# Performance work log

Hardware: AMD Instinct MI355X
Metric: run time of the kernel (lower is better)

Reference implementation:

```python
import jax, jax.numpy as jnp
import numpy as np

ENC_H = 512
DEC_H = 512
FIELD = 128

def setup_inputs() -> dict:
    key = jax.random.key(0)
    ks = jax.random.split(key, 12)
    B, S, T = 8, 256, 32
    def lin(k, fan_in, fan_out):
        k1, k2 = jax.random.split(k)
        bound = 1.0 / np.sqrt(fan_in)
        W = jax.random.uniform(k1, (fan_in, fan_out), minval=-bound, maxval=bound, dtype=jnp.float32)
        b = jax.random.uniform(k2, (fan_out,), minval=-bound, maxval=bound, dtype=jnp.float32)
        return W, b
    W1, b1 = lin(ks[0], ENC_H, DEC_H)
    W2, b2 = lin(ks[1], DEC_H, DEC_H)
    W3, b3 = lin(ks[2], FIELD, DEC_H)
    W4, b4 = lin(ks[3], DEC_H, DEC_H)
    return {
        "output": jax.random.normal(ks[4], (B, T, DEC_H), dtype=jnp.float32),
        "encoder_hidden": jax.random.normal(ks[5], (S, B, ENC_H), dtype=jnp.float32),
        "input_z": jax.random.normal(ks[6], (B, S, FIELD), dtype=jnp.float32),
        "W1": W1, "b1": b1, "W2": W2, "b2": b2,
        "W3": W3, "b3": b3, "W4": W4, "b4": b4,
    }

def reference(output, encoder_hidden, input_z, W1, b1, W2, b2, W3, b3, W4, b4):
    S, B, He = encoder_hidden.shape
    # tanh(lin1(encoder_hidden)) then .view(B, S, D)  (reshape, NOT transpose -- faithful to torch .view)
    out_hs = jnp.tanh(encoder_hidden @ W1 + b1).reshape(B, S, -1)      # [B,S,D]
    enc_h = encoder_hidden.reshape(B, S, He)                            # [B,S,He]
    out_fds = jnp.tanh(input_z @ W3 + b3)                               # [B,S,D]
    out2 = jnp.tanh(output @ W2 + b2)                                   # [B,T,D]
    out3 = jnp.tanh(output @ W4 + b4)                                   # [B,T,D]
    # vectorized over timesteps: g1[b,s,t,d] = out_hs[b,s,d]*out2[b,t,d]
    g1 = out_hs[:, :, None, :] * out2[:, None, :, :]                    # [B,S,T,D]
    alpha = jax.nn.softmax(g1, axis=1)                                  # softmax over S, per feature d
    g2 = out_fds[:, :, None, :] * out3[:, None, :, :]                   # [B,S,T,D]
    beta = jax.nn.softmax(g2, axis=1)
    q = alpha * beta                                                    # [B,S,T,D]
    qn = jax.lax.stop_gradient(jnp.sum(q, axis=1, keepdims=True))       # detached normalizer
    gamma = q / qn                                                      # [B,S,T,D]
    contex = jnp.sum(gamma * enc_h[:, :, None, :], axis=1)              # [B,T,D]
    concat_vectors = jnp.concatenate([output, contex], axis=-1)         # [B,T,2D]
    # attn: list over t of gamma[:, :, t, :] -> stacked [B,T,S,D]
    attn = jnp.transpose(gamma, (0, 2, 1, 3))
    return (concat_vectors, attn)
```

## Files before the change

### kernel.cpp

```cpp
#include <hip/hip_runtime.h>


typedef __attribute__((ext_vector_type(8))) short bf16x8;
typedef __attribute__((ext_vector_type(4))) float f32x4;

__device__ __forceinline__ unsigned short f2bf(float x) {
    union { float f; unsigned u; } v; v.f = x;
    unsigned r = v.u + 0x7fffu + ((v.u >> 16) & 1u);
    return (unsigned short)(r >> 16);
}

__global__ __launch_bounds__(256) void prep_k(
    const float* __restrict__ E, const float* __restrict__ Z, const float* __restrict__ O,
    const float* __restrict__ W1, const float* __restrict__ W2,
    const float* __restrict__ W3, const float* __restrict__ W4,
    unsigned short* __restrict__ Ebf, unsigned short* __restrict__ Zbf,
    unsigned short* __restrict__ Obf,
    unsigned short* __restrict__ W1T, unsigned short* __restrict__ W2T,
    unsigned short* __restrict__ W3T, unsigned short* __restrict__ W4T)
{
    int bid = blockIdx.x;
    if (bid < 1408) {
        const float* src; unsigned short* dst; int base;
        if (bid < 1024)      { src = E; dst = Ebf; base = bid; }
        else if (bid < 1280) { src = Z; dst = Zbf; base = bid - 1024; }
        else                 { src = O; dst = Obf; base = bid - 1280; }
        int i = base * 1024 + threadIdx.x * 4;
        float4 v = *(const float4*)(src + i);
        ushort4 r;
        r.x = f2bf(v.x); r.y = f2bf(v.y); r.z = f2bf(v.z); r.w = f2bf(v.w);
        *(ushort4*)(dst + i) = r;
        return;
    }
    int tb = bid - 1408;
    const float* W; unsigned short* WT; int K;
    if (tb < 256)      {            W = W1; WT = W1T; K = 512; }
    else if (tb < 512) { tb -= 256; W = W2; WT = W2T; K = 512; }
    else if (tb < 576) { tb -= 512; W = W3; WT = W3T; K = 128; }
    else               { tb -= 576; W = W4; WT = W4T; K = 512; }
    int n0 = (tb & 15) * 32;
    int k0 = (tb >> 4) * 32;
    __shared__ float tile[32][33];
    int tx = threadIdx.x & 31, ty = threadIdx.x >> 5;
    #pragma unroll
    for (int i = 0; i < 32; i += 8)
        tile[ty + i][tx] = W[(k0 + ty + i) * 512 + n0 + tx];
    __syncthreads();
    #pragma unroll
    for (int i = 0; i < 32; i += 8)
        WT[(n0 + ty + i) * K + k0 + tx] = f2bf(tile[tx][ty + i]);
}

__global__ __launch_bounds__(256) void gemm_all_k(
    const unsigned short* __restrict__ Ebf, const unsigned short* __restrict__ Zbf,
    const unsigned short* __restrict__ Obf,
    const unsigned short* __restrict__ W1T, const unsigned short* __restrict__ W3T,
    const unsigned short* __restrict__ W2T, const unsigned short* __restrict__ W4T,
    const float* __restrict__ b1, const float* __restrict__ b3,
    const float* __restrict__ b2, const float* __restrict__ b4,
    float* __restrict__ L1, float* __restrict__ F,
    float* __restrict__ O2, float* __restrict__ O3)
{
    int id = blockIdx.x;
    const unsigned short* A; const unsigned short* BT; const float* bias; float* C;
    int K;
    if (id < 256)      {             A = Ebf; BT = W1T; bias = b1; C = L1; K = 512; }
    else if (id < 512) { id -= 256;  A = Zbf; BT = W3T; bias = b3; C = F;  K = 128; }
    else if (id < 544) { id -= 512;  A = Obf; BT = W2T; bias = b2; C = O2; K = 512; }
    else               { id -= 544;  A = Obf; BT = W4T; bias = b4; C = O3; K = 512; }
    int m0 = (id >> 3) * 64;
    int n0 = (id & 7) * 64;

    __shared__ unsigned short As[64 * 72];
    __shared__ unsigned short Bs[64 * 72];

    int tid  = threadIdx.x;
    int wave = tid >> 6;
    int lane = tid & 63;
    int lm   = lane & 15;
    int lq   = lane >> 4;

    int srow = tid >> 2;
    int scol = (tid & 3) * 16;

    f32x4 acc[4];
    #pragma unroll
    for (int c = 0; c < 4; ++c) acc[c] = f32x4{0.f, 0.f, 0.f, 0.f};

    for (int k0 = 0; k0 < K; k0 += 64) {
        __syncthreads();
        const unsigned short* Ap = &A[(m0 + srow) * K + k0 + scol];
        const unsigned short* Bp = &BT[(n0 + srow) * K + k0 + scol];
        *(uint4*)(&As[srow * 72 + scol])     = *(const uint4*)(Ap);
        *(uint4*)(&As[srow * 72 + scol + 8]) = *(const uint4*)(Ap + 8);
        *(uint4*)(&Bs[srow * 72 + scol])     = *(const uint4*)(Bp);
        *(uint4*)(&Bs[srow * 72 + scol + 8]) = *(const uint4*)(Bp + 8);
        __syncthreads();
        #pragma unroll
        for (int ks = 0; ks < 2; ++ks) {
            bf16x8 af = *(const bf16x8*)(&As[(wave * 16 + lm) * 72 + ks * 32 + lq * 8]);
            #pragma unroll
            for (int c = 0; c < 4; ++c) {
                bf16x8 bfr = *(const bf16x8*)(&Bs[(c * 16 + lm) * 72 + ks * 32 + lq * 8]);
                acc[c] = __builtin_amdgcn_mfma_f32_16x16x32_bf16(af, bfr, acc[c], 0, 0, 0);
            }
        }
    }

    #pragma unroll
    for (int c = 0; c < 4; ++c) {
        int col = n0 + c * 16 + lm;
        float bv = bias[col];
        #pragma unroll
        for (int r = 0; r < 4; ++r) {
            int row = m0 + wave * 16 + lq * 4 + r;
            float x = acc[c][r] + bv;
            x = fminf(fmaxf(x, -15.f), 15.f);
            float t = __expf(2.0f * x);
            C[row * 512 + col] = (t - 1.0f) / (t + 1.0f);
        }
    }
}

__global__ __launch_bounds__(256) void attn_partial_k(
    const float* __restrict__ L1, const float* __restrict__ F,
    const float* __restrict__ O2, const float* __restrict__ O3,
    const float* __restrict__ Enc,
    float* __restrict__ sum_p, float* __restrict__ csum_p)
{
    int b  = blockIdx.x >> 4;
    int sc = blockIdx.x & 15;
    int tc = blockIdx.y;
    int d  = blockIdx.z * 256 + threadIdx.x;

    float c2[8], c3[8], sum[8], csum[8];
    #pragma unroll
    for (int i = 0; i < 8; ++i) {
        int bt = b * 32 + tc * 8 + i;
        c2[i] = O2[bt * 512 + d];
        c3[i] = O3[bt * 512 + d];
        sum[i] = 0.f; csum[i] = 0.f;
    }

    int s0 = sc * 16;
    const float* L1b = L1  + (b * 256 + s0) * 512 + d;
    const float* Fb  = F   + (b * 256 + s0) * 512 + d;
    const float* Eb  = Enc + (b * 256 + s0) * 512 + d;

    #pragma unroll 2
    for (int s = 0; s < 16; ++s) {
        float l1 = L1b[s * 512];
        float f  = Fb[s * 512];
        float eh = Eb[s * 512];
        #pragma unroll
        for (int i = 0; i < 8; ++i) {
            float e = __expf(l1 * c2[i] + f * c3[i]);
            sum[i]  += e;
            csum[i] += e * eh;
        }
    }

    #pragma unroll
    for (int i = 0; i < 8; ++i) {
        int idx = ((b * 16 + sc) * 32 + tc * 8 + i) * 512 + d;
        sum_p[idx]  = sum[i];
        csum_p[idx] = csum[i];
    }
}

__global__ __launch_bounds__(256) void attn_finalize_k(
    const float* __restrict__ sum_p, const float* __restrict__ csum_p,
    const float* __restrict__ Out,
    float* __restrict__ out0, float* __restrict__ invA)
{
    int bt = blockIdx.x;
    int d  = blockIdx.y * 256 + threadIdx.x;
    int b  = bt >> 5, t = bt & 31;

    float sum = 0.f, csum = 0.f;
    #pragma unroll
    for (int sc = 0; sc < 16; ++sc) {
        int idx = ((b * 16 + sc) * 32 + t) * 512 + d;
        sum  += sum_p[idx];
        csum += csum_p[idx];
    }
    float inv = 1.0f / sum;
    invA[bt * 512 + d] = inv;
    out0[bt * 1024 + d]       = Out[bt * 512 + d];
    out0[bt * 1024 + 512 + d] = csum * inv;
}

__global__ __launch_bounds__(256) void attn_write_k(
    const float* __restrict__ L1, const float* __restrict__ F,
    const float* __restrict__ O2, const float* __restrict__ O3,
    const float* __restrict__ invA,
    float* __restrict__ attn)
{
    int b     = blockIdx.x;
    int sbase = blockIdx.y * 8 + (threadIdx.x >> 7) * 4;
    int d4    = (threadIdx.x & 127) * 4;

    f32x4 l1[4], f[4];
    #pragma unroll
    for (int j = 0; j < 4; ++j) {
        l1[j] = *(const f32x4*)(L1 + (b * 256 + sbase + j) * 512 + d4);
        f[j]  = *(const f32x4*)(F  + (b * 256 + sbase + j) * 512 + d4);
    }

    for (int t = 0; t < 32; ++t) {
        int bt = b * 32 + t;
        f32x4 c2 = *(const f32x4*)(O2   + bt * 512 + d4);
        f32x4 c3 = *(const f32x4*)(O3   + bt * 512 + d4);
        f32x4 iv = *(const f32x4*)(invA + bt * 512 + d4);
        #pragma unroll
        for (int j = 0; j < 4; ++j) {
            f32x4 g;
            g[0] = __expf(l1[j][0] * c2[0] + f[j][0] * c3[0]) * iv[0];
            g[1] = __expf(l1[j][1] * c2[1] + f[j][1] * c3[1]) * iv[1];
            g[2] = __expf(l1[j][2] * c2[2] + f[j][2] * c3[2]) * iv[2];
            g[3] = __expf(l1[j][3] * c2[3] + f[j][3] * c3[3]) * iv[3];
            __builtin_nontemporal_store(
                g, (f32x4*)(attn + ((size_t)(bt * 256 + sbase + j)) * 512 + d4));
        }
    }
}

extern "C" void kernel_launch(void* const* d_in, const int* in_sizes, int n_in,
                              void* d_out, int out_size, void* d_ws, size_t ws_size,
                              hipStream_t stream)
{
    const float* Out = (const float*)d_in[0];
    const float* Enc = (const float*)d_in[1];
    const float* Z   = (const float*)d_in[2];
    const float* W1  = (const float*)d_in[3];
    const float* b1  = (const float*)d_in[4];
    const float* W2  = (const float*)d_in[5];
    const float* b2  = (const float*)d_in[6];
    const float* W3  = (const float*)d_in[7];
    const float* b3  = (const float*)d_in[8];
    const float* W4  = (const float*)d_in[9];
    const float* b4  = (const float*)d_in[10];

    char* ws = (char*)d_ws;
    size_t off = 0;
    auto alloc = [&](size_t n) -> char* {
        char* p = ws + off; off += (n + 255) & ~(size_t)255; return p;
    };
    unsigned short* Ebf = (unsigned short*)alloc(1048576 * 2);
    unsigned short* Zbf = (unsigned short*)alloc(262144 * 2);
    unsigned short* Obf = (unsigned short*)alloc(131072 * 2);
    unsigned short* W1T = (unsigned short*)alloc(262144 * 2);
    unsigned short* W2T = (unsigned short*)alloc(262144 * 2);
    unsigned short* W3T = (unsigned short*)alloc(65536 * 2);
    unsigned short* W4T = (unsigned short*)alloc(262144 * 2);
    float* L1    = (float*)alloc(1048576 * 4);
    float* F     = (float*)alloc(1048576 * 4);
    float* O2    = (float*)alloc(131072 * 4);
    float* O3    = (float*)alloc(131072 * 4);
    float* sum_p = (float*)alloc(2097152 * 4);
    float* csum_p= (float*)alloc(2097152 * 4);
    float* invA  = (float*)alloc(131072 * 4);

    float* out0 = (float*)d_out;
    float* attn = out0 + 262144;

    hipLaunchKernelGGL(prep_k, dim3(2240), dim3(256), 0, stream,
                       Enc, Z, Out, W1, W2, W3, W4,
                       Ebf, Zbf, Obf, W1T, W2T, W3T, W4T);
    hipLaunchKernelGGL(gemm_all_k, dim3(576), dim3(256), 0, stream,
                       Ebf, Zbf, Obf, W1T, W3T, W2T, W4T,
                       b1, b3, b2, b4, L1, F, O2, O3);
    hipLaunchKernelGGL(attn_partial_k, dim3(128, 4, 2), dim3(256), 0, stream,
                       L1, F, O2, O3, Enc, sum_p, csum_p);
    hipLaunchKernelGGL(attn_finalize_k, dim3(256, 2), dim3(256), 0, stream,
                       sum_p, csum_p, Out, out0, invA);
    hipLaunchKernelGGL(attn_write_k, dim3(8, 32), dim3(256), 0, stream,
                       L1, F, O2, O3, invA, attn);
}
```

Baseline: 202.6 us.

## Fuse attention partial, finalize and write kernels into one per-(b,t) kernel

Replaces the three-kernel attention pipeline (partial sums over S chunks, finalize, write) with one kernel per (batch, timestep, d-chunk). Each block reduces over all S with a shared-memory cross-wave reduction, computes the normalizer and context, then recomputes exp to write attn. This removes the partial-sum buffers and two launches. In exchange, L1/F/Enc are re-read per timestep and exp is computed twice.

```diff
diff --git a/kernel.cpp b/kernel.cpp
--- a/kernel.cpp
+++ b/kernel.cpp
@@ -122,106 +122,80 @@
     }
 }
 
-__global__ __launch_bounds__(256) void attn_partial_k(
+__global__ __launch_bounds__(256) void attn_fused_k(
     const float* __restrict__ L1, const float* __restrict__ F,
     const float* __restrict__ O2, const float* __restrict__ O3,
-    const float* __restrict__ Enc,
-    float* __restrict__ sum_p, float* __restrict__ csum_p)
-{
-    int b  = blockIdx.x >> 4;
-    int sc = blockIdx.x & 15;
-    int tc = blockIdx.y;
-    int d  = blockIdx.z * 256 + threadIdx.x;
-
-    float c2[8], c3[8], sum[8], csum[8];
-    #pragma unroll
-    for (int i = 0; i < 8; ++i) {
-        int bt = b * 32 + tc * 8 + i;
-        c2[i] = O2[bt * 512 + d];
-        c3[i] = O3[bt * 512 + d];
-        sum[i] = 0.f; csum[i] = 0.f;
-    }
-
-    int s0 = sc * 16;
-    const float* L1b = L1  + (b * 256 + s0) * 512 + d;
-    const float* Fb  = F   + (b * 256 + s0) * 512 + d;
-    const float* Eb  = Enc + (b * 256 + s0) * 512 + d;
-
-    #pragma unroll 2
-    for (int s = 0; s < 16; ++s) {
-        float l1 = L1b[s * 512];
-        float f  = Fb[s * 512];
-        float eh = Eb[s * 512];
+    const float* __restrict__ Enc, const float* __restrict__ Out,
+    float* __restrict__ out0, float* __restrict__ attn)
+{
+    int b  = blockIdx.x;
+    int t  = blockIdx.y;
+    int dc = blockIdx.z;
+    int bt = b * 32 + t;
+
+    int so = threadIdx.x >> 5;
+    int dq = threadIdx.x & 31;
+    int d4 = dc * 128 + dq * 4;
+
+    __shared__ f32x4 rsum[8][32];
+    __shared__ f32x4 rcsum[8][32];
+    __shared__ f32x4 ivs[32];
+
+    f32x4 c2 = *(const f32x4*)(O2 + bt * 512 + d4);
+    f32x4 c3 = *(const f32x4*)(O3 + bt * 512 + d4);
+
+    const float* L1b = L1  + b * 256 * 512 + d4;
+    const float* Fb  = F   + b * 256 * 512 + d4;
+    const float* Eb  = Enc + b * 256 * 512 + d4;
+
+    f32x4 sum = f32x4{0.f, 0.f, 0.f, 0.f};
+    f32x4 csum = f32x4{0.f, 0.f, 0.f, 0.f};
+    #pragma unroll 4
+    for (int s = so; s < 256; s += 8) {
+        f32x4 l1 = *(const f32x4*)(L1b + s * 512);
+        f32x4 f  = *(const f32x4*)(Fb  + s * 512);
+        f32x4 eh = *(const f32x4*)(Eb  + s * 512);
+        f32x4 e;
+        e[0] = __expf(l1[0] * c2[0] + f[0] * c3[0]);
+        e[1] = __expf(l1[1] * c2[1] + f[1] * c3[1]);
+        e[2] = __expf(l1[2] * c2[2] + f[2] * c3[2]);
+        e[3] = __expf(l1[3] * c2[3] + f[3] * c3[3]);
+        sum += e;
+        csum[0] += e[0] * eh[0]; csum[1] += e[1] * eh[1];
+        csum[2] += e[2] * eh[2]; csum[3] += e[3] * eh[3];
+    }
+    rsum[so][dq]  = sum;
+    rcsum[so][dq] = csum;
+    __syncthreads();
+
+    if (threadIdx.x < 32) {
+        f32x4 ts = rsum[0][dq], tc = rcsum[0][dq];
         #pragma unroll
-        for (int i = 0; i < 8; ++i) {
-            float e = __expf(l1 * c2[i] + f * c3[i]);
-            sum[i]  += e;
-            csum[i] += e * eh;
-        }
-    }
-
-    #pragma unroll
-    for (int i = 0; i < 8; ++i) {
-        int idx = ((b * 16 + sc) * 32 + tc * 8 + i) * 512 + d;
-        sum_p[idx]  = sum[i];
-        csum_p[idx] = csum[i];
-    }
-}
-
-__global__ __launch_bounds__(256) void attn_finalize_k(
-    const float* __restrict__ sum_p, const float* __restrict__ csum_p,
-    const float* __restrict__ Out,
-    float* __restrict__ out0, float* __restrict__ invA)
-{
-    int bt = blockIdx.x;
-    int d  = blockIdx.y * 256 + threadIdx.x;
-    int b  = bt >> 5, t = bt & 31;
-
-    float sum = 0.f, csum = 0.f;
-    #pragma unroll
-    for (int sc = 0; sc < 16; ++sc) {
-        int idx = ((b * 16 + sc) * 32 + t) * 512 + d;
-        sum  += sum_p[idx];
-        csum += csum_p[idx];
-    }
-    float inv = 1.0f / sum;
-    invA[bt * 512 + d] = inv;
-    out0[bt * 1024 + d]       = Out[bt * 512 + d];
-    out0[bt * 1024 + 512 + d] = csum * inv;
-}
-
-__global__ __launch_bounds__(256) void attn_write_k(
-    const float* __restrict__ L1, const float* __restrict__ F,
-    const float* __restrict__ O2, const float* __restrict__ O3,
-    const float* __restrict__ invA,
-    float* __restrict__ attn)
-{
-    int b     = blockIdx.x;
-    int sbase = blockIdx.y * 8 + (threadIdx.x >> 7) * 4;
-    int d4    = (threadIdx.x & 127) * 4;
-
-    f32x4 l1[4], f[4];
-    #pragma unroll
-    for (int j = 0; j < 4; ++j) {
-        l1[j] = *(const f32x4*)(L1 + (b * 256 + sbase + j) * 512 + d4);
-        f[j]  = *(const f32x4*)(F  + (b * 256 + sbase + j) * 512 + d4);
-    }
-
-    for (int t = 0; t < 32; ++t) {
-        int bt = b * 32 + t;
-        f32x4 c2 = *(const f32x4*)(O2   + bt * 512 + d4);
-        f32x4 c3 = *(const f32x4*)(O3   + bt * 512 + d4);
-        f32x4 iv = *(const f32x4*)(invA + bt * 512 + d4);
-        #pragma unroll
-        for (int j = 0; j < 4; ++j) {
-            f32x4 g;
-            g[0] = __expf(l1[j][0] * c2[0] + f[j][0] * c3[0]) * iv[0];
-            g[1] = __expf(l1[j][1] * c2[1] + f[j][1] * c3[1]) * iv[1];
-            g[2] = __expf(l1[j][2] * c2[2] + f[j][2] * c3[2]) * iv[2];
-            g[3] = __expf(l1[j][3] * c2[3] + f[j][3] * c3[3]) * iv[3];
-            __builtin_nontemporal_store(
-                g, (f32x4*)(attn + ((size_t)(bt * 256 + sbase + j)) * 512 + d4));
-        }
+        for (int j = 1; j < 8; ++j) { ts += rsum[j][dq]; tc += rcsum[j][dq]; }
+        f32x4 inv;
+        inv[0] = 1.0f / ts[0]; inv[1] = 1.0f / ts[1];
+        inv[2] = 1.0f / ts[2]; inv[3] = 1.0f / ts[3];
+        ivs[dq] = inv;
+        f32x4 ctx;
+        ctx[0] = tc[0] * inv[0]; ctx[1] = tc[1] * inv[1];
+        ctx[2] = tc[2] * inv[2]; ctx[3] = tc[3] * inv[3];
+        *(f32x4*)(out0 + bt * 1024 + 512 + d4) = ctx;
+        *(f32x4*)(out0 + bt * 1024 + d4) = *(const f32x4*)(Out + bt * 512 + d4);
+    }
+    __syncthreads();
+
+    f32x4 iv = ivs[dq];
+    float* ap = attn + (size_t)bt * 256 * 512 + d4;
+    #pragma unroll 4
+    for (int s = so; s < 256; s += 8) {
+        f32x4 l1 = *(const f32x4*)(L1b + s * 512);
+        f32x4 f  = *(const f32x4*)(Fb  + s * 512);
+        f32x4 g;
+        g[0] = __expf(l1[0] * c2[0] + f[0] * c3[0]) * iv[0];
+        g[1] = __expf(l1[1] * c2[1] + f[1] * c3[1]) * iv[1];
+        g[2] = __expf(l1[2] * c2[2] + f[2] * c3[2]) * iv[2];
+        g[3] = __expf(l1[3] * c2[3] + f[3] * c3[3]) * iv[3];
+        __builtin_nontemporal_store(g, (f32x4*)(ap + s * 512));
     }
 }
 
@@ -253,13 +227,10 @@
     unsigned short* W2T = (unsigned short*)alloc(262144 * 2);
     unsigned short* W3T = (unsigned short*)alloc(65536 * 2);
     unsigned short* W4T = (unsigned short*)alloc(262144 * 2);
-    float* L1    = (float*)alloc(1048576 * 4);
-    float* F     = (float*)alloc(1048576 * 4);
-    float* O2    = (float*)alloc(131072 * 4);
-    float* O3    = (float*)alloc(131072 * 4);
-    float* sum_p = (float*)alloc(2097152 * 4);
-    float* csum_p= (float*)alloc(2097152 * 4);
-    float* invA  = (float*)alloc(131072 * 4);
+    float* L1 = (float*)alloc(1048576 * 4);
+    float* F  = (float*)alloc(1048576 * 4);
+    float* O2 = (float*)alloc(131072 * 4);
+    float* O3 = (float*)alloc(131072 * 4);
 
     float* out0 = (float*)d_out;
     float* attn = out0 + 262144;
@@ -270,10 +241,6 @@
     hipLaunchKernelGGL(gemm_all_k, dim3(576), dim3(256), 0, stream,
                        Ebf, Zbf, Obf, W1T, W3T, W2T, W4T,
                        b1, b3, b2, b4, L1, F, O2, O3);
-    hipLaunchKernelGGL(attn_partial_k, dim3(128, 4, 2), dim3(256), 0, stream,
-                       L1, F, O2, O3, Enc, sum_p, csum_p);
-    hipLaunchKernelGGL(attn_finalize_k, dim3(256, 2), dim3(256), 0, stream,
-                       sum_p, csum_p, Out, out0, invA);
-    hipLaunchKernelGGL(attn_write_k, dim3(8, 32), dim3(256), 0, stream,
-                       L1, F, O2, O3, invA, attn);
-}
+    hipLaunchKernelGGL(attn_fused_k, dim3(8, 32, 4), dim3(256), 0, stream,
+                       L1, F, O2, O3, Enc, Out, out0, attn);
+}
```

Result: slower. 207.5 us (+2.4%).
